# Performance work log

Hardware: AMD Instinct MI355X
Metric: run time of the kernel (lower is better)

The kernel has to match this reference:

```python
import jax, jax.numpy as jnp
import numpy as np


def setup_inputs() -> dict:
    key = jax.random.key(0)
    k1, k2, k3, k4 = jax.random.split(key, 4)
    T, D_e, D_o, Hm, Wm = 16, 128, 512, 32, 32
    Bq, Hq, Wq = 4, 32, 32
    return {
        "m_in": jax.random.normal(k1, (T, D_e, Hm, Wm), dtype=jnp.float32),
        "m_out": jax.random.normal(k2, (T, D_o, Hm, Wm), dtype=jnp.float32),
        "q_in": jax.random.normal(k3, (Bq, D_e, Hq, Wq), dtype=jnp.float32),
        "q_out": jax.random.normal(k4, (Bq, D_o, Hq, Wq), dtype=jnp.float32),
    }


def reference(m_in, m_out, q_in, q_out):
    Bq, D_e, Hq, Wq = q_in.shape
    T, _, Hm, Wm = m_in.shape
    D_o = m_out.shape[1]
    N = T * Hm * Wm
    # Faithful to torch: raw reshape (no transpose of axes) of memory tensors.
    mi = m_in.reshape(D_e, N)            # [D_e, N]
    qi = q_in.reshape(Bq, D_e, Hq * Wq)  # [Bq, D_e, Q]
    # p[b, n, q] = sum_d mi[d, n] * qi[b, d, q]
    p = jnp.einsum("dn,bdq->bnq", mi, qi) / jnp.sqrt(jnp.asarray(D_e, q_in.dtype))
    p = jax.nn.softmax(p, axis=1)        # softmax over memory locations
    mo = m_out.reshape(D_o, N)           # [D_o, N]
    mem = jnp.einsum("on,bnq->boq", mo, p).reshape(Bq, D_o, Hq, Wq)
    mem_out = jnp.concatenate([mem, q_out], axis=1)  # [Bq, D_o + D_o, Hq, Wq]
    return (mem_out, p)
```

## Files before the change

kernel.cpp:

```cpp
#include <hip/hip_runtime.h>
#include <hip/hip_bf16.h>
#include <cstddef>


#define DE   128
#define DO   512
#define NMEM 16384
#define QCOL 1024

typedef __attribute__((ext_vector_type(8))) short    short8v;
typedef __attribute__((ext_vector_type(8))) _Float16 half8v;
typedef __attribute__((ext_vector_type(4))) float    f32x4;
typedef __attribute__((ext_vector_type(2))) float    f32x2;
typedef __attribute__((ext_vector_type(2))) unsigned u32x2;
typedef __attribute__((ext_vector_type(4))) unsigned u32x4;

__device__ __forceinline__ short f2bf(float x) {
    union { __hip_bfloat16 h; short s; } u;
    u.h = __float2bfloat16(x);
    return u.s;
}

__device__ __forceinline__ unsigned pk_fp8x4(float f0, float f1, float f2, float f3) {
    unsigned r = __builtin_amdgcn_cvt_pk_fp8_f32(f0, f1, 0, false);
    r = __builtin_amdgcn_cvt_pk_fp8_f32(f2, f3, r, true);
    return r;
}

#define FSW(r) ((((r) >> 3) ^ (r)) & 7)

__device__ __forceinline__ void gl16c(const unsigned char* g, unsigned char* l) {
    __builtin_amdgcn_global_load_lds(
        (const __attribute__((address_space(1))) void*)g,
        (__attribute__((address_space(3))) void*)l, 16, 0, 0);
}


__global__ __launch_bounds__(256, 2)
void k1_mfma(const float* __restrict__ mi, const float* __restrict__ qi,
             unsigned char* __restrict__ e8, float* __restrict__ partial)
{
    const int bid = blockIdx.x;
    const int c   = bid & 7;
    const int r   = bid >> 3;
    const int qt  = r & 7;
    const int g   = ((r >> 3) << 3) | c;
    const int nt  = g & 127;
    const int b   = g >> 7;
    const int qb  = qt << 7;
    const int nb  = nt << 7;

    __shared__ __align__(16) short AfBf[2][128 * 128];
    __shared__ float red2[2][128];

    short* Bq = AfBf[0];
    short* An = AfBf[1];
    unsigned char* T8 = (unsigned char*)AfBf[0];

    const int tid  = threadIdx.x;
    const int lane = tid & 63;
    const int w    = tid >> 6;
    const int wn2  = (w >> 1) << 6;
    const int wq   = (w & 1) << 6;
    const int la   = lane & 15;
    const int kg   = lane >> 4;

    {
        const int d8 = (tid >> 4) << 3;
        const int c4 = (tid & 15) << 2;
        const float* qib = qi + (size_t)b * (DE * QCOL) + (size_t)d8 * QCOL + qb;
        const float* mib = mi + (size_t)d8 * NMEM + nb;
#pragma unroll
        for (int half = 0; half < 2; ++half) {
            const int cc = c4 + (half << 6);
            f32x4 qv[8], mv[8];
#pragma unroll
            for (int i = 0; i < 8; ++i) {
                qv[i] = *(const f32x4*)(qib + (size_t)i * QCOL + cc);
                mv[i] = *(const f32x4*)(mib + (size_t)i * NMEM + cc);
            }
#pragma unroll
            for (int j = 0; j < 4; ++j) {
                const int row = cc + j;
                const int off = row * 128 + ((((d8 >> 3) ^ FSW(row))) << 3);
                half8v av, bv;
#pragma unroll
                for (int i = 0; i < 8; ++i) {
                    av[i] = (_Float16)qv[i][j];
                    bv[i] = (_Float16)mv[i][j];
                }
                *(half8v*)&Bq[off] = av;
                *(half8v*)&An[off] = bv;
            }
        }
    }
    __syncthreads();

    f32x4 acc[4][4];
#pragma unroll
    for (int i = 0; i < 4; ++i)
#pragma unroll
        for (int j = 0; j < 4; ++j) acc[i][j] = (f32x4){0.f, 0.f, 0.f, 0.f};

#pragma unroll
    for (int ks = 0; ks < 4; ++ks) {
        half8v af[4], bf[4];
#pragma unroll
        for (int f = 0; f < 4; ++f) {
            const int ra = wn2 + f * 16 + la;
            const int rb = wq  + f * 16 + la;
            af[f] = *(const half8v*)&An[ra * 128 + ((((ks << 2) + kg) ^ FSW(ra)) << 3)];
            bf[f] = *(const half8v*)&Bq[rb * 128 + ((((ks << 2) + kg) ^ FSW(rb)) << 3)];
        }
#pragma unroll
        for (int fm = 0; fm < 4; ++fm)
#pragma unroll
            for (int fn = 0; fn < 4; ++fn)
                acc[fm][fn] = __builtin_amdgcn_mfma_f32_16x16x32_f16(
                    af[fm], bf[fn], acc[fm][fn], 0, 0, 0);
    }

    const float scale = 0.08838834764831845f;
#pragma unroll
    for (int fm = 0; fm < 4; ++fm)
#pragma unroll
        for (int fn = 0; fn < 4; ++fn)
#pragma unroll
            for (int rr = 0; rr < 4; ++rr)
                acc[fm][fn][rr] = __expf(acc[fm][fn][rr] * scale);

    float val[4];
#pragma unroll
    for (int fn = 0; fn < 4; ++fn) {
        float s = 0.f;
#pragma unroll
        for (int fm = 0; fm < 4; ++fm)
#pragma unroll
            for (int rr = 0; rr < 4; ++rr) s += acc[fm][fn][rr];
        s += __shfl_xor(s, 16);
        s += __shfl_xor(s, 32);
        val[fn] = s;
    }

    __syncthreads();

#pragma unroll
    for (int fn = 0; fn < 4; ++fn) {
        const int q  = wq + fn * 16 + la;
        const int fq = FSW(q);
#pragma unroll
        for (int fm = 0; fm < 4; ++fm) {
            const int n0 = wn2 + fm * 16 + (kg << 2);
            const unsigned rv = pk_fp8x4(acc[fm][fn][0], acc[fm][fn][1],
                                         acc[fm][fn][2], acc[fm][fn][3]);
            *(unsigned*)&T8[q * 128 + (((n0 >> 4) ^ fq) << 4) + (n0 & 15)] = rv;
        }
    }
    if (kg == 0) {
#pragma unroll
        for (int fn = 0; fn < 4; ++fn)
            red2[w >> 1][wq + fn * 16 + la] = val[fn];
    }
    __syncthreads();

    if (tid < 128) {
        partial[(size_t)nt * 4096 + (b << 10) + qb + tid] =
            red2[0][tid] + red2[1][tid];
    }

    {
        const int ql = tid >> 1;
        const int h  = tid & 1;
        const int fq = FSW(ql);
        unsigned char* dst = e8 + ((size_t)b << 24) + (size_t)(qb + ql) * NMEM + nb;
#pragma unroll
        for (int k = 0; k < 4; ++k) {
            const int m = h * 4 + k;
            u32x4 v = *(const u32x4*)&T8[ql * 128 + ((m ^ fq) << 4)];
            *(u32x4*)(dst + m * 16) = v;
        }
    }
}

__global__ __launch_bounds__(256)
void k3_big(float* __restrict__ p, const unsigned char* __restrict__ e8,
            const float* __restrict__ invsum)
{
    const int qb = blockIdx.x << 6;
    const int nb = blockIdx.y << 7;
    const int b  = blockIdx.z;

    __shared__ __align__(16) float P[64 * 128];

    const int tid = threadIdx.x;

    {
        const int ql  = tid >> 2;
        const int nc  = (tid & 3) << 5;
        const int fq  = FSW(ql);
        const float inv = invsum[(b << 10) + qb + ql];
        const unsigned char* rowp = e8 + ((size_t)b << 24)
                                       + (size_t)(qb + ql) * NMEM + nb + nc;
#pragma unroll
        for (int k = 0; k < 4; ++k) {
            u32x2 v = *(const u32x2*)(rowp + k * 8);
            f32x2 d0 = __builtin_amdgcn_cvt_pk_f32_fp8(v[0], false);
            f32x2 d1 = __builtin_amdgcn_cvt_pk_f32_fp8(v[0], true);
            f32x2 d2 = __builtin_amdgcn_cvt_pk_f32_fp8(v[1], false);
            f32x2 d3 = __builtin_amdgcn_cvt_pk_f32_fp8(v[1], true);
            float f[8];
            f[0] = d0[0] * inv; f[1] = d0[1] * inv;
            f[2] = d1[0] * inv; f[3] = d1[1] * inv;
            f[4] = d2[0] * inv; f[5] = d2[1] * inv;
            f[6] = d3[0] * inv; f[7] = d3[1] * inv;
            const int gg0 = (nc >> 2) + k * 2;
            *(f32x4*)&P[ql * 128 + (((gg0)     ^ fq) << 2)] = *(f32x4*)&f[0];
            *(f32x4*)&P[ql * 128 + (((gg0 + 1) ^ fq) << 2)] = *(f32x4*)&f[4];
        }
    }
    __syncthreads();

    {
        const int tx  = tid & 15;
        const int tyy = tid >> 4;
        float* pb = p + ((size_t)b << 24);
#pragma unroll
        for (int rr = 0; rr < 2; ++rr) {
            const int gg = tyy + 16 * rr;
            f32x4 v[4];
#pragma unroll
            for (int i = 0; i < 4; ++i) {
                const int ql = tx * 4 + i;
                v[i] = *(const f32x4*)&P[ql * 128 + ((gg ^ FSW(ql)) << 2)];
            }
#pragma unroll
            for (int jj = 0; jj < 4; ++jj) {
                f32x4 o = {v[0][jj], v[1][jj], v[2][jj], v[3][jj]};
                *(f32x4*)(pb + (size_t)(nb + gg * 4 + jj) * QCOL + qb + tx * 4) = o;
            }
        }
    }
}

__global__ __launch_bounds__(256)
void conv8(const float* __restrict__ mo, unsigned char* __restrict__ mo8)
{
    const size_t u = (size_t)blockIdx.x * 256 + threadIdx.x;
#pragma unroll
    for (int r = 0; r < 4; ++r) {
        const size_t i = (u + (size_t)r * 262144) << 3;
        f32x4 a = *(const f32x4*)(mo + i);
        f32x4 c = *(const f32x4*)(mo + i + 4);
        u32x2 v;
        v[0] = pk_fp8x4(a[0], a[1], a[2], a[3]);
        v[1] = pk_fp8x4(c[0], c[1], c[2], c[3]);
        *(u32x2*)(mo8 + i) = v;
    }
}

__global__ __launch_bounds__(256, 2)
void k4_sk8(const unsigned char* __restrict__ mo8,
            const unsigned char* __restrict__ e8,
            float* __restrict__ out0, float* __restrict__ part)
{
    const int sw    = ((blockIdx.x & 7) << 6) | (blockIdx.x >> 3);
    const int split = sw >> 7;
    const int tile  = sw & 127;
    const int b  = tile >> 5;
    const int ot = (tile >> 3) & 3;
    const int qt = tile & 7;
    const int ob = ot << 7;
    const int qb = qt << 7;
    const int kb = split << 12;

    __shared__ __align__(16) unsigned char As[2][128 * 128];
    __shared__ __align__(16) unsigned char Bs[2][128 * 128];

    const int tid  = threadIdx.x;
    const int lane = tid & 63;
    const int w    = tid >> 6;
    const int wm   = (w >> 1) << 6;
    const int wn   = (w & 1) << 6;
    const int la   = lane & 15;
    const int kg   = lane >> 4;

    size_t offA[4], offB[4];
    int lbo[4];
#pragma unroll
    for (int i = 0; i < 4; ++i) {
        const int rb  = (w << 5) + (i << 3);
        const int row = rb + (lane >> 3);
        const int gs  = (lane & 7) ^ FSW(row);
        offA[i] = (size_t)(ob + row) * NMEM + gs * 16;
        offB[i] = (size_t)(qb + row) * NMEM + gs * 16;
        lbo[i]  = rb * 128;
    }
    const unsigned char* e8b = e8 + ((size_t)b << 24);

#define SK_STAGE(BUF, K0)                                                      \
    do {                                                                       \
        _Pragma("unroll")                                                      \
        for (int i = 0; i < 4; ++i) {                                          \
            gl16c(mo8 + offA[i] + (K0), &As[BUF][lbo[i]]);                     \
            gl16c(e8b + offB[i] + (K0), &Bs[BUF][lbo[i]]);                     \
        }                                                                      \
    } while (0)

    int rA[4][4], rB[4][4];
#pragma unroll
    for (int f = 0; f < 4; ++f) {
        const int rowA = wm + f * 16 + la;
        const int rowB = wn + f * 16 + la;
#pragma unroll
        for (int ks = 0; ks < 4; ++ks) {
            const int gg = ks * 2 + (kg >> 1);
            rA[f][ks] = rowA * 128 + ((gg ^ FSW(rowA)) << 4) + ((kg & 1) << 3);
            rB[f][ks] = rowB * 128 + ((gg ^ FSW(rowB)) << 4) + ((kg & 1) << 3);
        }
    }

    f32x4 acc[4][4];
#pragma unroll
    for (int i = 0; i < 4; ++i)
#pragma unroll
        for (int j = 0; j < 4; ++j) acc[i][j] = (f32x4){0.f, 0.f, 0.f, 0.f};

    SK_STAGE(0, kb);
    __syncthreads();

    int cur = 0;
    for (int t = 0; t < 32; ++t) {
        const bool pf = (t + 1) < 32;
        if (pf) SK_STAGE(cur ^ 1, kb + (t + 1) * 128);

#pragma unroll
        for (int ks = 0; ks < 4; ++ks) {
            long af[4], bf[4];
#pragma unroll
            for (int f = 0; f < 4; ++f) {
                af[f] = *(const long*)&As[cur][rA[f][ks]];
                bf[f] = *(const long*)&Bs[cur][rB[f][ks]];
            }
#pragma unroll
            for (int fm = 0; fm < 4; ++fm)
#pragma unroll
                for (int fn = 0; fn < 4; ++fn)
                    acc[fm][fn] = __builtin_amdgcn_mfma_f32_16x16x32_fp8_fp8(
                        af[fm], bf[fn], acc[fm][fn], 0, 0, 0);
        }
        __syncthreads();
        cur ^= 1;
    }

    if (split == 0) {
        float* outb = out0 + ((size_t)b << 20);
#pragma unroll
        for (int fm = 0; fm < 4; ++fm)
#pragma unroll
            for (int fn = 0; fn < 4; ++fn)
#pragma unroll
                for (int rr = 0; rr < 4; ++rr) {
                    const int o = ob + wm + fm * 16 + (kg << 2) + rr;
                    const int q = qb + wn + fn * 16 + la;
                    outb[(size_t)o * 1024 + q] = acc[fm][fn][rr];
                }
    } else {
        float* pp = part + (size_t)(split - 1) * 2097152;
#pragma unroll
        for (int fm = 0; fm < 4; ++fm)
#pragma unroll
            for (int fn = 0; fn < 4; ++fn)
#pragma unroll
                for (int rr = 0; rr < 4; ++rr) {
                    const int o = ob + wm + fm * 16 + (kg << 2) + rr;
                    const int q = qb + wn + fn * 16 + la;
                    pp[(((size_t)(b << 9) + o) << 10) + q] = acc[fm][fn][rr];
                }
    }
#undef SK_STAGE
}

__global__ __launch_bounds__(256)
void k56_fin(float* __restrict__ out0, const float* __restrict__ part,
             const float* __restrict__ invsum, const float* __restrict__ qo)
{
    const size_t t = (size_t)blockIdx.x * 256 + threadIdx.x;
    if (t < 524288ull) {
        const size_t v = t << 2;
        const int b = (int)(v >> 19);
        const int q = (int)(v & 1023);
        float* dst = out0 + v + ((size_t)b << 19);
        f32x4 s0 = *(const f32x4*)dst;
        f32x4 s1 = *(const f32x4*)(part + v);
        f32x4 s2 = *(const f32x4*)(part + v + 2097152);
        f32x4 s3 = *(const f32x4*)(part + v + 4194304);
        f32x4 inv = *(const f32x4*)(invsum + (b << 10) + q);
        f32x4 o;
#pragma unroll
        for (int h = 0; h < 4; ++h)
            o[h] = (s0[h] + s1[h] + s2[h] + s3[h]) * inv[h];
        *(f32x4*)dst = o;
        const f32x4 cv = *(const f32x4*)(qo + v);
        *(f32x4*)(out0 + v + ((size_t)(b + 1) << 19)) = cv;
    }
}


__global__ __launch_bounds__(256, 2)
void k1_p(const float* __restrict__ mi, const float* __restrict__ qi,
          float* __restrict__ p, float* __restrict__ partial)
{
    const int qb = blockIdx.x << 7;
    const int nb = blockIdx.y << 7;
    const int b  = blockIdx.z;
    const float* __restrict__ qib = qi + (size_t)b * (DE * QCOL);

    __shared__ float As[8][132];
    __shared__ float Bs[8][132];
    __shared__ float red[16][128];

    const int tid = threadIdx.x;
    const int tx  = tid & 15;
    const int ty  = tid >> 4;

    float acc[8][8];
#pragma unroll
    for (int i = 0; i < 8; ++i)
#pragma unroll
        for (int j = 0; j < 8; ++j) acc[i][j] = 0.f;

    const int ld_d = tid >> 5;
    const int ld_n = (tid & 31) << 2;

    for (int k0 = 0; k0 < DE; k0 += 8) {
        float4 av = *(const float4*)(mi  + (size_t)(k0 + ld_d) * NMEM + nb + ld_n);
        float4 bv = *(const float4*)(qib + (size_t)(k0 + ld_d) * QCOL + qb + ld_n);
        *(float4*)&As[ld_d][ld_n] = av;
        *(float4*)&Bs[ld_d][ld_n] = bv;
        __syncthreads();
#pragma unroll
        for (int kk = 0; kk < 8; ++kk) {
            float a[8], bb[8];
            *(float4*)&a[0]  = *(float4*)&As[kk][ty * 8];
            *(float4*)&a[4]  = *(float4*)&As[kk][ty * 8 + 4];
            *(float4*)&bb[0] = *(float4*)&Bs[kk][tx * 8];
            *(float4*)&bb[4] = *(float4*)&Bs[kk][tx * 8 + 4];
#pragma unroll
            for (int i = 0; i < 8; ++i)
#pragma unroll
                for (int j = 0; j < 8; ++j)
                    acc[i][j] += a[i] * bb[j];
        }
        __syncthreads();
    }

    const float scale = 0.08838834764831845f;
    float cs[8];
#pragma unroll
    for (int j = 0; j < 8; ++j) cs[j] = 0.f;
    float* __restrict__ pb = p + ((size_t)b << 24);
#pragma unroll
    for (int i = 0; i < 8; ++i) {
        const int n = nb + ty * 8 + i;
        float e[8];
#pragma unroll
        for (int j = 0; j < 8; ++j) {
            e[j] = __expf(acc[i][j] * scale);
            cs[j] += e[j];
        }
        *(float4*)(pb + ((size_t)n << 10) + qb + tx * 8)     = *(float4*)&e[0];
        *(float4*)(pb + ((size_t)n << 10) + qb + tx * 8 + 4) = *(float4*)&e[4];
    }

#pragma unroll
    for (int j = 0; j < 8; ++j) red[ty][tx * 8 + j] = cs[j];
    __syncthreads();
    if (tid < 128) {
        float s = 0.f;
#pragma unroll
        for (int t = 0; t < 16; ++t) s += red[t][tid];
        partial[(size_t)blockIdx.y * 4096 + (b << 10) + qb + tid] = s;
    }
}

__global__ __launch_bounds__(256)
void k3_small(float* __restrict__ p, const float* __restrict__ invsum)
{
    const size_t stride = (size_t)gridDim.x * blockDim.x;
    for (size_t t = (size_t)blockIdx.x * 256 + threadIdx.x; t < 16777216ull; t += stride) {
        const size_t i = t << 2;
        float4 v = *(float4*)(p + i);
        const int q = (int)(i & 1023);
        const int b = (int)(i >> 24);
        const float4 inv = *(const float4*)(invsum + (b << 10) + q);
        v.x *= inv.x; v.y *= inv.y; v.z *= inv.z; v.w *= inv.w;
        *(float4*)(p + i) = v;
    }
}

__global__ __launch_bounds__(256, 2)
void k4_reg(const float* __restrict__ mo, const float* __restrict__ p,
            float* __restrict__ out0)
{
    const int qb = blockIdx.x << 6;
    const int ob = blockIdx.y << 6;
    const int b  = blockIdx.z;
    const float* __restrict__ pb = p + ((size_t)b << 24);

    __shared__ __align__(16) short As[2][64 * 128];
    __shared__ __align__(16) short Bs[2][64 * 128];

    const int tid  = threadIdx.x;
    const int lane = tid & 63;
    const int w    = tid >> 6;
    const int wm   = (w >> 1) << 5;
    const int wn   = (w & 1) << 5;

    const int aro = tid >> 4;
    const int ak8 = (tid & 15) << 3;
    const int bn8 = (tid >> 4) << 3;
    const int bq4 = (tid & 15) << 2;

    int sA[4], sB[4];
#pragma unroll
    for (int j = 0; j < 4; ++j) {
        const int rlA = aro + 16 * j;
        sA[j] = rlA * 128 + ((((ak8 >> 3) ^ FSW(rlA))) << 3);
        const int rlB = bq4 + j;
        sB[j] = rlB * 128 + ((((bn8 >> 3) ^ FSW(rlB))) << 3);
    }

    const float* __restrict__ gA = mo + (size_t)(ob + aro) * NMEM + ak8;
    const float* __restrict__ gB = pb + (size_t)bn8 * QCOL + qb + bq4;

    f32x4 aA[4][2], aB[8];

#define K4_LOAD(K0)                                                              \
    do {                                                                         \
        _Pragma("unroll")                                                        \
        for (int j = 0; j < 4; ++j) {                                            \
            aA[j][0] = *(const f32x4*)(gA + (size_t)(16 * j) * NMEM + (K0));     \
            aA[j][1] = *(const f32x4*)(gA + (size_t)(16 * j) * NMEM + (K0) + 4); \
        }                                                                        \
        _Pragma("unroll")                                                        \
        for (int i = 0; i < 8; ++i)                                              \
            aB[i] = *(const f32x4*)(gB + ((size_t)(K0) + i) * QCOL);             \
    } while (0)

#define K4_STORE(BUF)                                                            \
    do {                                                                         \
        _Pragma("unroll")                                                        \
        for (int j = 0; j < 4; ++j) {                                            \
            short8v v;                                                           \
            _Pragma("unroll")                                                    \
            for (int h = 0; h < 4; ++h) { v[h] = f2bf(aA[j][0][h]);              \
                                          v[h + 4] = f2bf(aA[j][1][h]); }        \
            *(short8v*)&As[BUF][sA[j]] = v;                                      \
        }                                                                        \
        _Pragma("unroll")                                                        \
        for (int j = 0; j < 4; ++j) {                                            \
            short8v v;                                                           \
            _Pragma("unroll")                                                    \
            for (int i = 0; i < 8; ++i) v[i] = f2bf(aB[i][j]);                   \
            *(short8v*)&Bs[BUF][sB[j]] = v;                                      \
        }                                                                        \
    } while (0)

    f32x4 acc[2][2];
#pragma unroll
    for (int i = 0; i < 2; ++i)
#pragma unroll
        for (int j = 0; j < 2; ++j) acc[i][j] = (f32x4){0.f, 0.f, 0.f, 0.f};

    K4_LOAD(0);
    K4_STORE(0);
    __syncthreads();

    const int la = lane & 15;
    const int kg = lane >> 4;

    int rA[2][4], rB[2][4];
#pragma unroll
    for (int fm = 0; fm < 2; ++fm) {
        const int rowA = wm + la + 16 * fm;
        const int rowB = wn + la + 16 * fm;
#pragma unroll
        for (int s = 0; s < 4; ++s) {
            rA[fm][s] = rowA * 128 + ((((s << 2) + kg) ^ FSW(rowA)) << 3);
            rB[fm][s] = rowB * 128 + ((((s << 2) + kg) ^ FSW(rowB)) << 3);
        }
    }

    int cur = 0;
    for (int t = 0; t < NMEM / 128; ++t) {
        const bool pf = (t + 1) < NMEM / 128;
        if (pf) K4_LOAD((t + 1) * 128);

#pragma unroll
        for (int s = 0; s < 4; ++s) {
            short8v a0 = *(const short8v*)&As[cur][rA[0][s]];
            short8v a1 = *(const short8v*)&As[cur][rA[1][s]];
            short8v b0 = *(const short8v*)&Bs[cur][rB[0][s]];
            short8v b1 = *(const short8v*)&Bs[cur][rB[1][s]];
            acc[0][0] = __builtin_amdgcn_mfma_f32_16x16x32_bf16(a0, b0, acc[0][0], 0, 0, 0);
            acc[0][1] = __builtin_amdgcn_mfma_f32_16x16x32_bf16(a0, b1, acc[0][1], 0, 0, 0);
            acc[1][0] = __builtin_amdgcn_mfma_f32_16x16x32_bf16(a1, b0, acc[1][0], 0, 0, 0);
            acc[1][1] = __builtin_amdgcn_mfma_f32_16x16x32_bf16(a1, b1, acc[1][1], 0, 0, 0);
        }

        if (pf) K4_STORE(cur ^ 1);
        __syncthreads();
        cur ^= 1;
    }

    const int orow = ob + wm + (kg << 2);
    const int qcol = qb + wn + la;
    float* __restrict__ outb = out0 + ((size_t)b << 20);
#pragma unroll
    for (int fm = 0; fm < 2; ++fm)
#pragma unroll
        for (int fn = 0; fn < 2; ++fn)
#pragma unroll
            for (int r = 0; r < 4; ++r)
                outb[(size_t)(orow + 16 * fm + r) * 1024 + qcol + 16 * fn] =
                    acc[fm][fn][r];
#undef K4_LOAD
#undef K4_STORE
}

__global__ __launch_bounds__(256)
void k5_copy(const float* __restrict__ qo, float* __restrict__ out0)
{
    const size_t t = (size_t)blockIdx.x * 256 + threadIdx.x;
    if (t < 524288ull) {
        const size_t i = t << 2;
        const size_t b = i >> 19;
        const float4 v = *(const float4*)(qo + i);
        *(float4*)(out0 + i + ((b + 1) << 19)) = v;
    }
}


__global__ __launch_bounds__(256)
void k2b_red(const float* __restrict__ partial, float* __restrict__ invsum)
{
    __shared__ float red[8][32];
    const int col = blockIdx.x * 32 + (threadIdx.x & 31);
    const int g   = threadIdx.x >> 5;
    float s = 0.f;
#pragma unroll
    for (int r = 0; r < 16; ++r)
        s += partial[(size_t)(g * 16 + r) * 4096 + col];
    red[g][threadIdx.x & 31] = s;
    __syncthreads();
    if (threadIdx.x < 32) {
        float t = 0.f;
#pragma unroll
        for (int g2 = 0; g2 < 8; ++g2) t += red[g2][threadIdx.x];
        invsum[col] = 1.0f / t;
    }
}

extern "C" void kernel_launch(void* const* d_in, const int* in_sizes, int n_in,
                              void* d_out, int out_size, void* d_ws, size_t ws_size,
                              hipStream_t stream)
{
    const float* m_in  = (const float*)d_in[0];
    const float* m_out = (const float*)d_in[1];
    const float* q_in  = (const float*)d_in[2];
    const float* q_out = (const float*)d_in[3];

    float* out0 = (float*)d_out;
    float* p    = out0 + 4194304;

    unsigned char* e8  = (unsigned char*)d_ws;
    unsigned char* mo8 = e8 + 67108864;
    float* wpart   = (float*)(e8 + 75497472);
    float* partialW= (float*)(e8 + 100663296);
    float* invsumW = (float*)(e8 + 102760448);

    float* partialF = out0 + 524288;
    float* invsumF  = out0 + 1048576 + 524288;

    const size_t need_big = 176160768ull;

    if (ws_size >= need_big) {
        conv8  <<<dim3(1024),       256, 0, stream>>>(m_out, mo8);
        k1_mfma<<<dim3(4096),       256, 0, stream>>>(m_in, q_in, e8, partialW);
        k2b_red<<<dim3(128),        256, 0, stream>>>(partialW, invsumW);
        k3_big <<<dim3(16, 128, 4), 256, 0, stream>>>(p, e8, invsumW);
        k4_sk8 <<<dim3(512),        256, 0, stream>>>(mo8, e8, out0, wpart);
        k56_fin<<<dim3(2048),       256, 0, stream>>>(out0, wpart, invsumW, q_out);
    } else {
        k1_p    <<<dim3(8, 128, 4), 256, 0, stream>>>(m_in, q_in, p, partialF);
        k2b_red <<<dim3(128),       256, 0, stream>>>(partialF, invsumF);
        k3_small<<<dim3(2048),      256, 0, stream>>>(p, invsumF);
        k4_reg  <<<dim3(16, 8, 4),  256, 0, stream>>>(m_out, p, out0);
        k5_copy <<<dim3(2048),      256, 0, stream>>>(q_out, out0);
    }
}
```

Measured before the change: 192.5 us.

## Fuse p-normalization and split-K GEMM into one interleaved launch

Merges the kernel that writes the normalized p tensor with the split-K FP8 GEMM into a single launch. Every 17th block does a GEMM tile and the rest do p-write tiles, so the bandwidth-bound p store overlaps the MFMA-bound GEMM. The GEMM's K step is halved to 64 with 32KB of shared memory, which allows occupancy of 4 blocks per CU. In exchange it doubles the number of barrier iterations and makes GEMM blocks share CUs with store-heavy blocks, which may lengthen the tail.

Measured after the change: 208.9 us. +8.5%, slower.

```diff
diff --git a/kernel.cpp b/kernel.cpp
--- a/kernel.cpp
+++ b/kernel.cpp
@@ -183,66 +183,6 @@
 }
 
 __global__ __launch_bounds__(256)
-void k3_big(float* __restrict__ p, const unsigned char* __restrict__ e8,
-            const float* __restrict__ invsum)
-{
-    const int qb = blockIdx.x << 6;
-    const int nb = blockIdx.y << 7;
-    const int b  = blockIdx.z;
-
-    __shared__ __align__(16) float P[64 * 128];
-
-    const int tid = threadIdx.x;
-
-    {
-        const int ql  = tid >> 2;
-        const int nc  = (tid & 3) << 5;
-        const int fq  = FSW(ql);
-        const float inv = invsum[(b << 10) + qb + ql];
-        const unsigned char* rowp = e8 + ((size_t)b << 24)
-                                       + (size_t)(qb + ql) * NMEM + nb + nc;
-#pragma unroll
-        for (int k = 0; k < 4; ++k) {
-            u32x2 v = *(const u32x2*)(rowp + k * 8);
-            f32x2 d0 = __builtin_amdgcn_cvt_pk_f32_fp8(v[0], false);
-            f32x2 d1 = __builtin_amdgcn_cvt_pk_f32_fp8(v[0], true);
-            f32x2 d2 = __builtin_amdgcn_cvt_pk_f32_fp8(v[1], false);
-            f32x2 d3 = __builtin_amdgcn_cvt_pk_f32_fp8(v[1], true);
-            float f[8];
-            f[0] = d0[0] * inv; f[1] = d0[1] * inv;
-            f[2] = d1[0] * inv; f[3] = d1[1] * inv;
-            f[4] = d2[0] * inv; f[5] = d2[1] * inv;
-            f[6] = d3[0] * inv; f[7] = d3[1] * inv;
-            const int gg0 = (nc >> 2) + k * 2;
-            *(f32x4*)&P[ql * 128 + (((gg0)     ^ fq) << 2)] = *(f32x4*)&f[0];
-            *(f32x4*)&P[ql * 128 + (((gg0 + 1) ^ fq) << 2)] = *(f32x4*)&f[4];
-        }
-    }
-    __syncthreads();
-
-    {
-        const int tx  = tid & 15;
-        const int tyy = tid >> 4;
-        float* pb = p + ((size_t)b << 24);
-#pragma unroll
-        for (int rr = 0; rr < 2; ++rr) {
-            const int gg = tyy + 16 * rr;
-            f32x4 v[4];
-#pragma unroll
-            for (int i = 0; i < 4; ++i) {
-                const int ql = tx * 4 + i;
-                v[i] = *(const f32x4*)&P[ql * 128 + ((gg ^ FSW(ql)) << 2)];
-            }
-#pragma unroll
-            for (int jj = 0; jj < 4; ++jj) {
-                f32x4 o = {v[0][jj], v[1][jj], v[2][jj], v[3][jj]};
-                *(f32x4*)(pb + (size_t)(nb + gg * 4 + jj) * QCOL + qb + tx * 4) = o;
-            }
-        }
-    }
-}
-
-__global__ __launch_bounds__(256)
 void conv8(const float* __restrict__ mo, unsigned char* __restrict__ mo8)
 {
     const size_t u = (size_t)blockIdx.x * 256 + threadIdx.x;
@@ -258,126 +198,190 @@
     }
 }
 
-__global__ __launch_bounds__(256, 2)
-void k4_sk8(const unsigned char* __restrict__ mo8,
-            const unsigned char* __restrict__ e8,
-            float* __restrict__ out0, float* __restrict__ part)
-{
-    const int sw    = ((blockIdx.x & 7) << 6) | (blockIdx.x >> 3);
-    const int split = sw >> 7;
-    const int tile  = sw & 127;
-    const int b  = tile >> 5;
-    const int ot = (tile >> 3) & 3;
-    const int qt = tile & 7;
-    const int ob = ot << 7;
-    const int qb = qt << 7;
-    const int kb = split << 12;
-
-    __shared__ __align__(16) unsigned char As[2][128 * 128];
-    __shared__ __align__(16) unsigned char Bs[2][128 * 128];
-
-    const int tid  = threadIdx.x;
-    const int lane = tid & 63;
-    const int w    = tid >> 6;
-    const int wm   = (w >> 1) << 6;
-    const int wn   = (w & 1) << 6;
-    const int la   = lane & 15;
-    const int kg   = lane >> 4;
-
-    size_t offA[4], offB[4];
-    int lbo[4];
-#pragma unroll
-    for (int i = 0; i < 4; ++i) {
-        const int rb  = (w << 5) + (i << 3);
-        const int row = rb + (lane >> 3);
-        const int gs  = (lane & 7) ^ FSW(row);
-        offA[i] = (size_t)(ob + row) * NMEM + gs * 16;
-        offB[i] = (size_t)(qb + row) * NMEM + gs * 16;
-        lbo[i]  = rb * 128;
-    }
-    const unsigned char* e8b = e8 + ((size_t)b << 24);
+__global__ __launch_bounds__(256, 4)
+void k34_fused(const unsigned char* __restrict__ mo8,
+               const unsigned char* __restrict__ e8,
+               const float* __restrict__ invsum,
+               float* __restrict__ p,
+               float* __restrict__ out0, float* __restrict__ part)
+{
+    __shared__ __align__(16) unsigned char SMEM[32768];
+
+    const int bid = blockIdx.x;
+    const int tid = threadIdx.x;
+
+    if (bid % 17 == 0) {
+        const int k4id  = bid / 17;
+        const int split = k4id >> 7;
+        const int tile  = k4id & 127;
+        const int b  = tile >> 5;
+        const int ot = (tile >> 3) & 3;
+        const int qt = tile & 7;
+        const int ob = ot << 7;
+        const int qb = qt << 7;
+        const int kb = split << 12;
+
+        unsigned char* As = SMEM;
+        unsigned char* Bs = SMEM + 16384;
+
+        const int lane = tid & 63;
+        const int w    = tid >> 6;
+        const int wm   = (w >> 1) << 6;
+        const int wn   = (w & 1) << 6;
+        const int la   = lane & 15;
+        const int kg   = lane >> 4;
+
+        size_t offA[2], offB[2];
+        int lbo[2];
+#pragma unroll
+        for (int i = 0; i < 2; ++i) {
+            const int rb  = (w << 5) + (i << 4);
+            const int row = rb + (lane >> 2);
+            const int gs  = (lane & 3) ^ (FSW(row) & 3);
+            offA[i] = (size_t)(ob + row) * NMEM + gs * 16;
+            offB[i] = (size_t)(qb + row) * NMEM + gs * 16;
+            lbo[i]  = rb * 64;
+        }
+        const unsigned char* e8b = e8 + ((size_t)b << 24);
 
 #define SK_STAGE(BUF, K0)                                                      \
-    do {                                                                       \
-        _Pragma("unroll")                                                      \
-        for (int i = 0; i < 4; ++i) {                                          \
-            gl16c(mo8 + offA[i] + (K0), &As[BUF][lbo[i]]);                     \
-            gl16c(e8b + offB[i] + (K0), &Bs[BUF][lbo[i]]);                     \
-        }                                                                      \
-    } while (0)
-
-    int rA[4][4], rB[4][4];
-#pragma unroll
-    for (int f = 0; f < 4; ++f) {
-        const int rowA = wm + f * 16 + la;
-        const int rowB = wn + f * 16 + la;
-#pragma unroll
-        for (int ks = 0; ks < 4; ++ks) {
-            const int gg = ks * 2 + (kg >> 1);
-            rA[f][ks] = rowA * 128 + ((gg ^ FSW(rowA)) << 4) + ((kg & 1) << 3);
-            rB[f][ks] = rowB * 128 + ((gg ^ FSW(rowB)) << 4) + ((kg & 1) << 3);
-        }
-    }
-
-    f32x4 acc[4][4];
-#pragma unroll
-    for (int i = 0; i < 4; ++i)
-#pragma unroll
-        for (int j = 0; j < 4; ++j) acc[i][j] = (f32x4){0.f, 0.f, 0.f, 0.f};
-
-    SK_STAGE(0, kb);
-    __syncthreads();
-
-    int cur = 0;
-    for (int t = 0; t < 32; ++t) {
-        const bool pf = (t + 1) < 32;
-        if (pf) SK_STAGE(cur ^ 1, kb + (t + 1) * 128);
-
-#pragma unroll
-        for (int ks = 0; ks < 4; ++ks) {
-            long af[4], bf[4];
-#pragma unroll
-            for (int f = 0; f < 4; ++f) {
-                af[f] = *(const long*)&As[cur][rA[f][ks]];
-                bf[f] = *(const long*)&Bs[cur][rB[f][ks]];
+        do {                                                                   \
+            _Pragma("unroll")                                                  \
+            for (int i = 0; i < 2; ++i) {                                      \
+                gl16c(mo8 + offA[i] + (K0), &As[(BUF) * 8192 + lbo[i]]);       \
+                gl16c(e8b + offB[i] + (K0), &Bs[(BUF) * 8192 + lbo[i]]);       \
+            }                                                                  \
+        } while (0)
+
+        int rA[4][2], rB[4][2];
+#pragma unroll
+        for (int f = 0; f < 4; ++f) {
+            const int rowA = wm + f * 16 + la;
+            const int rowB = wn + f * 16 + la;
+#pragma unroll
+            for (int ks = 0; ks < 2; ++ks) {
+                const int gg = ks * 2 + (kg >> 1);
+                rA[f][ks] = rowA * 64 + (((gg ^ (FSW(rowA) & 3))) << 4) + ((kg & 1) << 3);
+                rB[f][ks] = rowB * 64 + (((gg ^ (FSW(rowB) & 3))) << 4) + ((kg & 1) << 3);
             }
+        }
+
+        f32x4 acc[4][4];
+#pragma unroll
+        for (int i = 0; i < 4; ++i)
+#pragma unroll
+            for (int j = 0; j < 4; ++j) acc[i][j] = (f32x4){0.f, 0.f, 0.f, 0.f};
+
+        SK_STAGE(0, kb);
+        __syncthreads();
+
+        int cur = 0;
+        for (int t = 0; t < 64; ++t) {
+            const bool pf = (t + 1) < 64;
+            if (pf) SK_STAGE(cur ^ 1, kb + (t + 1) * 64);
+
+#pragma unroll
+            for (int ks = 0; ks < 2; ++ks) {
+                long af[4], bf[4];
+#pragma unroll
+                for (int f = 0; f < 4; ++f) {
+                    af[f] = *(const long*)&As[cur * 8192 + rA[f][ks]];
+                    bf[f] = *(const long*)&Bs[cur * 8192 + rB[f][ks]];
+                }
+#pragma unroll
+                for (int fm = 0; fm < 4; ++fm)
+#pragma unroll
+                    for (int fn = 0; fn < 4; ++fn)
+                        acc[fm][fn] = __builtin_amdgcn_mfma_f32_16x16x32_fp8_fp8(
+                            af[fm], bf[fn], acc[fm][fn], 0, 0, 0);
+            }
+            __syncthreads();
+            cur ^= 1;
+        }
+
+        if (split == 0) {
+            float* outb = out0 + ((size_t)b << 20);
 #pragma unroll
             for (int fm = 0; fm < 4; ++fm)
 #pragma unroll
                 for (int fn = 0; fn < 4; ++fn)
-                    acc[fm][fn] = __builtin_amdgcn_mfma_f32_16x16x32_fp8_fp8(
-                        af[fm], bf[fn], acc[fm][fn], 0, 0, 0);
+#pragma unroll
+                    for (int rr = 0; rr < 4; ++rr) {
+                        const int o = ob + wm + fm * 16 + (kg << 2) + rr;
+                        const int q = qb + wn + fn * 16 + la;
+                        outb[(size_t)o * 1024 + q] = acc[fm][fn][rr];
+                    }
+        } else {
+            float* pp = part + (size_t)(split - 1) * 2097152;
+#pragma unroll
+            for (int fm = 0; fm < 4; ++fm)
+#pragma unroll
+                for (int fn = 0; fn < 4; ++fn)
+#pragma unroll
+                    for (int rr = 0; rr < 4; ++rr) {
+                        const int o = ob + wm + fm * 16 + (kg << 2) + rr;
+                        const int q = qb + wn + fn * 16 + la;
+                        pp[(((size_t)(b << 9) + o) << 10) + q] = acc[fm][fn][rr];
+                    }
+        }
+#undef SK_STAGE
+    } else {
+        const int k3id = bid - bid / 17 - 1;
+        const int qt = k3id & 15;
+        const int nt = (k3id >> 4) & 127;
+        const int b  = k3id >> 11;
+        const int qb = qt << 6;
+        const int nb = nt << 7;
+
+        float* P = (float*)SMEM;
+
+        {
+            const int ql  = tid >> 2;
+            const int nc  = (tid & 3) << 5;
+            const int fq  = FSW(ql);
+            const float inv = invsum[(b << 10) + qb + ql];
+            const unsigned char* rowp = e8 + ((size_t)b << 24)
+                                           + (size_t)(qb + ql) * NMEM + nb + nc;
+#pragma unroll
+            for (int k = 0; k < 4; ++k) {
+                u32x2 v = *(const u32x2*)(rowp + k * 8);
+                f32x2 d0 = __builtin_amdgcn_cvt_pk_f32_fp8(v[0], false);
+                f32x2 d1 = __builtin_amdgcn_cvt_pk_f32_fp8(v[0], true);
+                f32x2 d2 = __builtin_amdgcn_cvt_pk_f32_fp8(v[1], false);
+                f32x2 d3 = __builtin_amdgcn_cvt_pk_f32_fp8(v[1], true);
+                float f[8];
+                f[0] = d0[0] * inv; f[1] = d0[1] * inv;
+                f[2] = d1[0] * inv; f[3] = d1[1] * inv;
+                f[4] = d2[0] * inv; f[5] = d2[1] * inv;
+                f[6] = d3[0] * inv; f[7] = d3[1] * inv;
+                const int gg0 = (nc >> 2) + k * 2;
+                *(f32x4*)&P[ql * 128 + (((gg0)     ^ fq) << 2)] = *(f32x4*)&f[0];
+                *(f32x4*)&P[ql * 128 + (((gg0 + 1) ^ fq) << 2)] = *(f32x4*)&f[4];
+            }
         }
         __syncthreads();
-        cur ^= 1;
-    }
-
-    if (split == 0) {
-        float* outb = out0 + ((size_t)b << 20);
-#pragma unroll
-        for (int fm = 0; fm < 4; ++fm)
-#pragma unroll
-            for (int fn = 0; fn < 4; ++fn)
-#pragma unroll
-                for (int rr = 0; rr < 4; ++rr) {
-                    const int o = ob + wm + fm * 16 + (kg << 2) + rr;
-                    const int q = qb + wn + fn * 16 + la;
-                    outb[(size_t)o * 1024 + q] = acc[fm][fn][rr];
+
+        {
+            const int tx  = tid & 15;
+            const int tyy = tid >> 4;
+            float* pb = p + ((size_t)b << 24);
+#pragma unroll
+            for (int rr = 0; rr < 2; ++rr) {
+                const int gg = tyy + 16 * rr;
+                f32x4 v[4];
+#pragma unroll
+                for (int i = 0; i < 4; ++i) {
+                    const int ql = tx * 4 + i;
+                    v[i] = *(const f32x4*)&P[ql * 128 + ((gg ^ FSW(ql)) << 2)];
                 }
-    } else {
-        float* pp = part + (size_t)(split - 1) * 2097152;
-#pragma unroll
-        for (int fm = 0; fm < 4; ++fm)
-#pragma unroll
-            for (int fn = 0; fn < 4; ++fn)
-#pragma unroll
-                for (int rr = 0; rr < 4; ++rr) {
-                    const int o = ob + wm + fm * 16 + (kg << 2) + rr;
-                    const int q = qb + wn + fn * 16 + la;
-                    pp[(((size_t)(b << 9) + o) << 10) + q] = acc[fm][fn][rr];
+#pragma unroll
+                for (int jj = 0; jj < 4; ++jj) {
+                    f32x4 o = {v[0][jj], v[1][jj], v[2][jj], v[3][jj]};
+                    *(f32x4*)(pb + (size_t)(nb + gg * 4 + jj) * QCOL + qb + tx * 4) = o;
                 }
-    }
-#undef SK_STAGE
+            }
+        }
+    }
 }
 
 __global__ __launch_bounds__(256)
@@ -685,12 +689,11 @@
     const size_t need_big = 176160768ull;
 
     if (ws_size >= need_big) {
-        conv8  <<<dim3(1024),       256, 0, stream>>>(m_out, mo8);
-        k1_mfma<<<dim3(4096),       256, 0, stream>>>(m_in, q_in, e8, partialW);
-        k2b_red<<<dim3(128),        256, 0, stream>>>(partialW, invsumW);
-        k3_big <<<dim3(16, 128, 4), 256, 0, stream>>>(p, e8, invsumW);
-        k4_sk8 <<<dim3(512),        256, 0, stream>>>(mo8, e8, out0, wpart);
-        k56_fin<<<dim3(2048),       256, 0, stream>>>(out0, wpart, invsumW, q_out);
+        conv8    <<<dim3(1024), 256, 0, stream>>>(m_out, mo8);
+        k1_mfma  <<<dim3(4096), 256, 0, stream>>>(m_in, q_in, e8, partialW);
+        k2b_red  <<<dim3(128),  256, 0, stream>>>(partialW, invsumW);
+        k34_fused<<<dim3(8704), 256, 0, stream>>>(mo8, e8, invsumW, p, out0, wpart);
+        k56_fin  <<<dim3(2048), 256, 0, stream>>>(out0, wpart, invsumW, q_out);
     } else {
         k1_p    <<<dim3(8, 128, 4), 256, 0, stream>>>(m_in, q_in, p, partialF);
         k2b_red <<<dim3(128),       256, 0, stream>>>(partialF, invsumF);
```
